# Kernel optimization log

Hardware: AMD Instinct MI355X
Metric: run time of the kernel (lower is better)

The kernel has to match this reference:

```python
import jax, jax.numpy as jnp
import numpy as np

D = 64      # in_feats
OUT = 64    # out_feats
MEM = 4     # mem_size
NREL = 8    # num_rels
N = 20000   # num nodes
E = 50000   # num edges
FF = 16     # dim_feedforward (hardcoded in module)
NH = 4      # nhead (hardcoded)
EPS = 1e-5  # LayerNorm eps (torch default)


def _ln(x, w, b):
    m = x.mean(-1, keepdims=True)
    v = ((x - m) ** 2).mean(-1, keepdims=True)
    return (x - m) * jax.lax.rsqrt(v + EPS) * w + b


def _enc(x, Wqkv, bqkv, Wo, bo, W1, b1, W2, b2, ln1w, ln1b, ln2w, ln2b):
    # torch TransformerEncoderLayer, batch_first, post-norm, eval mode, no padding mask (all-zero mask)
    B, S, d = x.shape
    dh = d // NH
    qkv = x @ Wqkv.T + bqkv
    q, k, v = jnp.split(qkv, 3, axis=-1)
    q = q.reshape(B, S, NH, dh)
    k = k.reshape(B, S, NH, dh)
    v = v.reshape(B, S, NH, dh)
    att = jax.nn.softmax(jnp.einsum('bqhd,bkhd->bhqk', q, k) / jnp.sqrt(jnp.float32(dh)), axis=-1)
    o = jnp.einsum('bhqk,bkhd->bqhd', att, v).reshape(B, S, d) @ Wo.T + bo
    x = _ln(x + o, ln1w, ln1b)
    ff = jax.nn.relu(x @ W1.T + b1) @ W2.T + b2
    return _ln(x + ff, ln2w, ln2b)


def setup_inputs() -> dict:
    key = jax.random.key(0)
    ks = jax.random.split(key, 16)
    s = 0.05
    inp = {
        'feat': jax.random.normal(ks[0], (N, D), jnp.float32),
        'src_idx': jax.random.randint(ks[1], (E,), 0, N),
        'dst_idx': jax.random.randint(ks[2], (E,), 0, N),
        'etype': jax.random.randint(ks[3], (E,), 0, NREL),
        'Wqkv': jax.random.normal(ks[4], (3 * D, D), jnp.float32) * s,
        'bqkv': jnp.zeros((3 * D,), jnp.float32),
        'Wo': jax.random.normal(ks[5], (D, D), jnp.float32) * s,
        'bo': jnp.zeros((D,), jnp.float32),
        'W1': jax.random.normal(ks[6], (FF, D), jnp.float32) * s,
        'b1': jnp.zeros((FF,), jnp.float32),
        'W2': jax.random.normal(ks[7], (D, FF), jnp.float32) * s,
        'b2': jnp.zeros((D,), jnp.float32),
        'ln1w': jnp.ones((D,), jnp.float32),
        'ln1b': jnp.zeros((D,), jnp.float32),
        'ln2w': jnp.ones((D,), jnp.float32),
        'ln2b': jnp.zeros((D,), jnp.float32),
        'Wc': jax.random.normal(ks[8], (MEM, D), jnp.float32) * s,
        'bc': jnp.zeros((MEM,), jnp.float32),
        'CLS': jax.random.normal(ks[9], (MEM, D), jnp.float32),
        'SEP': jax.random.normal(ks[10], (D,), jnp.float32),
        'Wm': jax.random.normal(ks[11], (OUT * D, D), jnp.float32) * s,
        'h_bias': jnp.zeros((OUT,), jnp.float32),
    }
    return inp


def reference(feat, src_idx, dst_idx, etype, Wqkv, bqkv, Wo, bo, W1, b1, W2, b2,
              ln1w, ln1b, ln2w, ln2b, Wc, bc, CLS, SEP, Wm, h_bias):
    enc_args = (Wqkv, bqkv, Wo, bo, W1, b1, W2, b2, ln1w, ln1b, ln2w, ln2b)

    def cls_pass(s_, d_):
        # run the shared encoder MEM times with a different CLS token; the math
        # is identical for every relation type, so no per-etype partition needed
        B = s_.shape[0]
        outs = []
        mem = jnp.zeros((B, D), s_.dtype)
        for i in range(MEM):
            cls = jnp.broadcast_to(CLS[i], (B, D))[:, None, :]
            sep = jnp.broadcast_to(SEP, (B, D))[:, None, :]
            seq = jnp.concatenate([cls, s_[:, None, :], sep, d_[:, None, :]], axis=1)  # [B,4,D]
            t = _enc(seq, *enc_args)[:, 0, :]
            outs.append(t)
            mem = mem + t
        return mem, jnp.stack(outs)  # [B,D], [MEM,B,D]

    src = feat[src_idx]  # [E,D]
    dst = feat[dst_idx]
    mem_emb, tmps = cls_pass(src, dst)
    cat_all = tmps @ Wc.T + bc               # [MEM,E,MEM]
    w = (mem_emb @ Wm.T).reshape(E, OUT, D)  # per-edge hypernetwork weight
    msg = jnp.einsum('eoi,ei->eo', w, src)   # [E,OUT]

    # dgl fn.mean aggregation over destination nodes (0 for isolated nodes)
    cnt = jax.ops.segment_sum(jnp.ones((E,), msg.dtype), dst_idx, num_segments=N)
    agg = jax.ops.segment_sum(msg, dst_idx, num_segments=N)
    node_rep = jnp.where(cnt[:, None] > 0, agg / jnp.maximum(cnt, 1.0)[:, None], 0.0)
    node_rep = node_rep + h_bias

    # self loop (same hypernetwork path over every node)
    mem_s, _ = cls_pass(feat, feat)
    hs = (mem_s @ Wm.T).reshape(N, OUT, D)
    node_rep = node_rep + jnp.einsum('noi,ni->no', hs, feat)

    # reconstruct torch concat order of category/label: outer loop etype, inner loop mem idx
    et = etype.astype(jnp.int32)
    counts = jax.ops.segment_sum(jnp.ones((E,), jnp.int32), etype, num_segments=NREL)
    start = jnp.concatenate([jnp.zeros((1,), jnp.int32), jnp.cumsum(counts)[:-1].astype(jnp.int32)])
    order = jnp.argsort(etype, stable=True)
    rank = jnp.zeros((E,), jnp.int32).at[order].set(jnp.arange(E, dtype=jnp.int32) - start[et[order]])
    base = start[et] * MEM + rank                                            # [E]
    pos = base[None, :] + jnp.arange(MEM, dtype=jnp.int32)[:, None] * counts[et][None, :]  # [MEM,E]
    category = jnp.zeros((MEM * E, MEM), cat_all.dtype).at[pos.reshape(-1)].set(cat_all.reshape(-1, MEM))
    label = jnp.zeros((MEM * E,), jnp.int32).at[pos.reshape(-1)].set(
        jnp.repeat(jnp.arange(MEM, dtype=jnp.int32), E))
    return node_rep, label, category
```

## Files before the change

kernel.cpp:

```cpp
#include <hip/hip_runtime.h>
#include <hip/hip_bf16.h>

typedef float f32x4_t __attribute__((ext_vector_type(4)));
typedef short bf16x8_t __attribute__((ext_vector_type(8)));

#define MFMA(a, b, c) __builtin_amdgcn_mfma_f32_16x16x32_bf16(a, b, c, 0, 0, 0)

#define C_Q0   0
#define C_S00  256
#define C_S02  272
#define C_VCLS 288
#define C_VSEP 544

__device__ __forceinline__ short f2bf(float x) {
    return (short)__builtin_bit_cast(unsigned short, __float2bfloat16(x));
}
__device__ __forceinline__ float bf2f(short s) {
    return __builtin_bit_cast(float, ((unsigned)(unsigned short)s) << 16);
}
__device__ __forceinline__ float head_sum16(float v) {
#pragma unroll
    for (int off = 1; off < 16; off <<= 1) v += __shfl_xor(v, off, 64);
    return v;
}

__global__ void k_prep(const float* __restrict__ Wo, const float* __restrict__ Wqkv,
                       const float* __restrict__ W1, const float* __restrict__ W2,
                       const float* __restrict__ Wm, const float* __restrict__ Wc,
                       const float* __restrict__ bqkv,
                       const float* __restrict__ CLS, const float* __restrict__ SEP,
                       const int* __restrict__ etype, const int* __restrict__ dst,
                       short* __restrict__ Bpack, short* __restrict__ WoP,
                       short* __restrict__ WkvP, short* __restrict__ W1P,
                       short* __restrict__ W2P, short* __restrict__ WcP,
                       float* __restrict__ consts,
                       int* __restrict__ hist, int* __restrict__ cnt, int E)
{
    int bx = blockIdx.x;
    if (bx < 136) {
        int tid = bx * 256 + threadIdx.x;
        short tmp[8];
        if (tid < 32768) {
            int u = tid, lane = u & 63, nt = (u >> 6) & 3, kstep = u >> 8;
            int o = nt * 16 + (lane & 15);
            int kb = kstep * 32 + (lane >> 4) * 8;
#pragma unroll
            for (int t = 0; t < 8; t++) { int k = kb + t; tmp[t] = f2bf(Wm[(o * 64 + (k >> 6)) * 64 + (k & 63)]); }
            *(bf16x8_t*)&Bpack[(size_t)u * 8] = *(bf16x8_t*)tmp;
        } else if (tid < 33280) {
            int u = tid - 32768, lane = u & 63, nt = (u >> 6) & 3, kstep = u >> 8;
            int o = nt * 16 + (lane & 15), kb = kstep * 32 + (lane >> 4) * 8;
#pragma unroll
            for (int t = 0; t < 8; t++) tmp[t] = f2bf(Wo[o * 64 + kb + t]);
            *(bf16x8_t*)&WoP[(size_t)u * 8] = *(bf16x8_t*)tmp;
        } else if (tid < 34304) {
            int u = tid - 33280, lane = u & 63, nt = (u >> 6) & 7, kstep = u >> 9;
            int col = nt * 16 + (lane & 15), kb = kstep * 32 + (lane >> 4) * 8;
            int row = 64 + col;
#pragma unroll
            for (int t = 0; t < 8; t++) tmp[t] = f2bf(Wqkv[row * 64 + kb + t]);
            *(bf16x8_t*)&WkvP[(size_t)u * 8] = *(bf16x8_t*)tmp;
        } else if (tid < 34432) {
            int u = tid - 34304, lane = u & 63, kstep = u >> 6;
            int f = lane & 15, kb = kstep * 32 + (lane >> 4) * 8;
#pragma unroll
            for (int t = 0; t < 8; t++) tmp[t] = f2bf(W1[f * 64 + kb + t]);
            *(bf16x8_t*)&W1P[(size_t)u * 8] = *(bf16x8_t*)tmp;
        } else if (tid < 34688) {
            int u = tid - 34432, lane = u & 63, nt = u >> 6;
            int o = nt * 16 + (lane & 15), kb = (lane >> 4) * 8;
#pragma unroll
            for (int t = 0; t < 8; t++) { int k = kb + t; tmp[t] = (k < 16) ? f2bf(W2[o * 16 + k]) : (short)0; }
            *(bf16x8_t*)&W2P[(size_t)u * 8] = *(bf16x8_t*)tmp;
        } else if (tid < 34816) {
            int u = tid - 34688, lane = u & 63, kstep = u >> 6;
            int m = lane & 15, kb = kstep * 32 + (lane >> 4) * 8;
#pragma unroll
            for (int t = 0; t < 8; t++) tmp[t] = (m < 4) ? f2bf(Wc[m * 64 + kb + t]) : (short)0;
            *(bf16x8_t*)&WcP[(size_t)u * 8] = *(bf16x8_t*)tmp;
        }
    } else if (bx == 136) {
        if (threadIdx.x < 64) {
            int lane = threadIdx.x;
            float ksep = bqkv[64 + lane], vsep = bqkv[128 + lane];
            for (int c = 0; c < 64; c++) {
                float sc = SEP[c];
                ksep += Wqkv[(64 + lane) * 64 + c] * sc;
                vsep += Wqkv[(128 + lane) * 64 + c] * sc;
            }
            consts[C_VSEP + lane] = vsep;
            for (int i = 0; i < 4; i++) {
                float q0 = bqkv[lane], kcls = bqkv[64 + lane], vcls = bqkv[128 + lane];
                for (int c = 0; c < 64; c++) {
                    float cc = CLS[i * 64 + c];
                    q0   += Wqkv[lane * 64 + c] * cc;
                    kcls += Wqkv[(64 + lane) * 64 + c] * cc;
                    vcls += Wqkv[(128 + lane) * 64 + c] * cc;
                }
                consts[C_Q0 + i * 64 + lane] = q0;
                consts[C_VCLS + i * 64 + lane] = vcls;
                float p00 = head_sum16(q0 * kcls) * 0.25f;
                float p02 = head_sum16(q0 * ksep) * 0.25f;
                if ((lane & 15) == 0) {
                    consts[C_S00 + i * 4 + (lane >> 4)] = p00;
                    consts[C_S02 + i * 4 + (lane >> 4)] = p02;
                }
            }
        }
    } else {
        __shared__ int h[8];
        int chunk = bx - 137;
        int tid = threadIdx.x;
        if (tid < 8) h[tid] = 0;
        __syncthreads();
        int e = chunk * 256 + tid;
        if (e < E) {
            atomicAdd(&h[etype[e]], 1);
            atomicAdd(&cnt[dst[e]], 1);
        }
        __syncthreads();
        if (tid < 8) hist[chunk * 8 + tid] = h[tid];
    }
}

__global__ void k_scan(const int* __restrict__ hist, int* __restrict__ chunkoff,
                       int* __restrict__ startg, int* __restrict__ countsg, int nch,
                       const float* __restrict__ consts, const float* __restrict__ Wqkv,
                       const float* __restrict__ bqkv,
                       short* __restrict__ WqkP, float* __restrict__ bqk)
{
    int lane = threadIdx.x;
    int g = lane & 7, seg = lane >> 3;
    int per = (nch + 7) / 8;
    int c0 = seg * per, c1 = c0 + per; if (c1 > nch) c1 = nch;
    int sum = 0;
    for (int c = c0; c < c1; c++) sum += hist[c * 8 + g];
    int pre = 0, tot = 0;
#pragma unroll
    for (int s2 = 0; s2 < 8; s2++) {
        int v = __shfl(sum, s2 * 8 + g, 64);
        tot += v;
        if (s2 < seg) pre += v;
    }
    int run = pre;
    for (int c = c0; c < c1; c++) { chunkoff[c * 8 + g] = run; run += hist[c * 8 + g]; }
    if (seg == 0) {
        countsg[g] = tot;
        int sg = 0;
#pragma unroll
        for (int g2 = 0; g2 < 8; g2++) { int v = __shfl(tot, g2, 64); if (g2 < g) sg += v; }
        startg[g] = sg;
    }

    int ih = lane & 15, ii = ih & 3, hh = ih >> 2;
    int lh8 = (lane >> 4) * 8;
    short tmp[8];
#pragma unroll
    for (int kstep = 0; kstep < 2; kstep++) {
#pragma unroll
        for (int t = 0; t < 8; t++) {
            int k = kstep * 32 + lh8 + t;
            float s = 0.f;
            for (int u = 0; u < 16; u++)
                s += consts[C_Q0 + ii * 64 + hh * 16 + u] * Wqkv[(64 + hh * 16 + u) * 64 + k];
            tmp[t] = f2bf(0.25f * s);
        }
        *(bf16x8_t*)&WqkP[(size_t)(kstep * 64 + lane) * 8] = *(bf16x8_t*)tmp;
    }
    if (lane < 16) {
        float s = 0.f;
        for (int u = 0; u < 16; u++)
            s += consts[C_Q0 + ii * 64 + hh * 16 + u] * bqkv[64 + hh * 16 + u];
        bqk[lane] = 0.25f * s;
    }
}

__global__ __launch_bounds__(256) void k_kv(const float* __restrict__ feat,
        const short* __restrict__ WkvP, const short* __restrict__ WqkP,
        const float* __restrict__ bqkv, const float* __restrict__ bqk,
        float* __restrict__ vnode, float* __restrict__ qs, int N)
{
    __shared__ __align__(16) short sA[64 * 72];
    int tid = threadIdx.x, lane = tid & 63, w = tid >> 6;
    int l15 = lane & 15, lh = lane >> 4;
    int base = blockIdx.x * 64;
#pragma unroll
    for (int rr = 0; rr < 16; rr++) {
        int row = w * 16 + rr;
        int n = base + row; n = n < N ? n : N - 1;
        sA[row * 72 + lane] = f2bf(feat[(size_t)n * 64 + lane]);
    }
    __syncthreads();
    const bf16x8_t* bp = (const bf16x8_t*)WkvP;
    bf16x8_t bv0 = bp[(0 * 8 + 4 + w) * 64 + lane];
    bf16x8_t bv1 = bp[(1 * 8 + 4 + w) * 64 + lane];
    bf16x8_t bq0 = ((const bf16x8_t*)WqkP)[lane];
    bf16x8_t bq1 = ((const bf16x8_t*)WqkP)[64 + lane];
    int kof = lh * 8;
    int col = w * 16 + l15;
    float biasv = bqkv[128 + col];
    float bqv = bqk[l15];
#pragma unroll
    for (int rt = 0; rt < 4; rt++) {
        bf16x8_t a0 = *(const bf16x8_t*)&sA[(rt * 16 + l15) * 72 + kof];
        bf16x8_t a1 = *(const bf16x8_t*)&sA[(rt * 16 + l15) * 72 + 32 + kof];
        f32x4_t av = {0.f, 0.f, 0.f, 0.f};
        av = MFMA(a0, bv0, av); av = MFMA(a1, bv1, av);
#pragma unroll
        for (int r = 0; r < 4; r++) {
            int n = base + rt * 16 + lh * 4 + r;
            if (n < N) vnode[(size_t)n * 64 + col] = av[r] + biasv;
        }
        if (w == 0) {
            f32x4_t aq = {0.f, 0.f, 0.f, 0.f};
            aq = MFMA(a0, bq0, aq); aq = MFMA(a1, bq1, aq);
#pragma unroll
            for (int r = 0; r < 4; r++) {
                int n = base + rt * 16 + lh * 4 + r;
                if (n < N) qs[(size_t)n * 16 + l15] = aq[r] + bqv;
            }
        }
    }
}

struct EncW {
    const float* consts; const float* CLS; const float* bo;
    const float* b1; const float* b2;
    const float* ln1w; const float* ln1b; const float* ln2w; const float* ln2b;
    const short* WoP; const short* W1P; const short* W2P; const short* WcP;
    const float* bc;
};

__global__ __launch_bounds__(256) void k_enc(const int* __restrict__ src_idx,
        const int* __restrict__ dst_idx,
        const float* __restrict__ vnode, const float* __restrict__ qs, EncW W,
        float* __restrict__ mem_out, float* __restrict__ cat_out, int E, int M)
{
    __shared__ __align__(16) short sA[64 * 72];
    __shared__ __align__(16) short sF[64 * 40];
    int tid = threadIdx.x, lane = tid & 63, w = tid >> 6;
    int l15 = lane & 15, lh = lane >> 4;
    int base = blockIdx.x * 16;

#pragma unroll
    for (int z = 0; z < 4; z++) {
        int zz = z * 64 + lane;
        sF[(w * 16 + (zz >> 4)) * 40 + 16 + (zz & 15)] = 0;
    }

    float vclsr[4], s00r[4], s02r[4];
#pragma unroll
    for (int i = 0; i < 4; i++) {
        vclsr[i] = W.consts[C_VCLS + i * 64 + lane];
        s00r[i]  = W.consts[C_S00 + i * 4 + lh];
        s02r[i]  = W.consts[C_S02 + i * 4 + lh];
    }
    float vsep = W.consts[C_VSEP + lane];

#pragma unroll
    for (int el = 0; el < 4; el++) {
        int eloc = w * 4 + el;
        int ge = base + eloc; int gc = ge < M ? ge : M - 1;
        int s, d;
        if (gc < E) { s = src_idx[gc]; d = dst_idx[gc]; }
        else        { s = gc - E; d = s; }
        float vs_ = vnode[(size_t)s * 64 + lane];
        float vd  = vnode[(size_t)d * 64 + lane];
        float4 qh_s = *(const float4*)&qs[(size_t)s * 16 + lh * 4];
        float4 qh_d = *(const float4*)&qs[(size_t)d * 16 + lh * 4];
        float qsv[4] = {qh_s.x, qh_s.y, qh_s.z, qh_s.w};
        float qdv[4] = {qh_d.x, qh_d.y, qh_d.z, qh_d.w};
#pragma unroll
        for (int i = 0; i < 4; i++) {
            float s01 = qsv[i], s03 = qdv[i];
            float s00 = s00r[i], s02 = s02r[i];
            float mx = fmaxf(fmaxf(s00, s01), fmaxf(s02, s03));
            float e0 = __expf(s00 - mx), e1 = __expf(s01 - mx);
            float e2 = __expf(s02 - mx), e3 = __expf(s03 - mx);
            float inv = 1.0f / (e0 + e1 + e2 + e3);
            float att = (e0 * vclsr[i] + e1 * vs_ + e2 * vsep + e3 * vd) * inv;
            sA[(eloc * 4 + i) * 72 + lane] = f2bf(att);
        }
    }

    int arow = (w * 16 + l15) * 72;
    int kof = lh * 8;

    const bf16x8_t* bpo = (const bf16x8_t*)W.WoP;
    f32x4_t ac0 = {0.f,0.f,0.f,0.f}, ac1 = ac0, ac2 = ac0, ac3 = ac0;
#pragma unroll
    for (int kstep = 0; kstep < 2; kstep++) {
        bf16x8_t a = *(const bf16x8_t*)&sA[arow + kstep * 32 + kof];
        ac0 = MFMA(a, bpo[(kstep * 4 + 0) * 64 + lane], ac0);
        ac1 = MFMA(a, bpo[(kstep * 4 + 1) * 64 + lane], ac1);
        ac2 = MFMA(a, bpo[(kstep * 4 + 2) * 64 + lane], ac2);
        ac3 = MFMA(a, bpo[(kstep * 4 + 3) * 64 + lane], ac3);
    }

    float x[4][4], y[4][4];
#pragma unroll
    for (int r = 0; r < 4; r++) { x[0][r] = ac0[r]; x[1][r] = ac1[r]; x[2][r] = ac2[r]; x[3][r] = ac3[r]; }
    float lw1[4], lb1[4];
#pragma unroll
    for (int nt = 0; nt < 4; nt++) {
        float b = W.bo[nt * 16 + l15];
        lw1[nt] = W.ln1w[nt * 16 + l15]; lb1[nt] = W.ln1b[nt * 16 + l15];
#pragma unroll
        for (int r = 0; r < 4; r++) x[nt][r] += b + W.CLS[r * 64 + nt * 16 + l15];
    }
#pragma unroll
    for (int r = 0; r < 4; r++) {
        float sm = head_sum16(x[0][r] + x[1][r] + x[2][r] + x[3][r]);
        float mu = sm * 0.015625f;
        float vv = 0.f;
#pragma unroll
        for (int nt = 0; nt < 4; nt++) { float dd = x[nt][r] - mu; vv = fmaf(dd, dd, vv); }
        vv = head_sum16(vv);
        float rs = rsqrtf(vv * 0.015625f + 1e-5f);
#pragma unroll
        for (int nt = 0; nt < 4; nt++) y[nt][r] = (x[nt][r] - mu) * rs * lw1[nt] + lb1[nt];
    }
#pragma unroll
    for (int nt = 0; nt < 4; nt++)
#pragma unroll
        for (int r = 0; r < 4; r++)
            sA[(w * 16 + lh * 4 + r) * 72 + nt * 16 + l15] = f2bf(y[nt][r]);

    const bf16x8_t* bp1 = (const bf16x8_t*)W.W1P;
    f32x4_t fa = {0.f,0.f,0.f,0.f};
#pragma unroll
    for (int kstep = 0; kstep < 2; kstep++) {
        bf16x8_t a = *(const bf16x8_t*)&sA[arow + kstep * 32 + kof];
        fa = MFMA(a, bp1[kstep * 64 + lane], fa);
    }
    float b1v = W.b1[l15];
#pragma unroll
    for (int r = 0; r < 4; r++)
        sF[(w * 16 + lh * 4 + r) * 40 + l15] = f2bf(fmaxf(fa[r] + b1v, 0.f));

    const bf16x8_t* bp2 = (const bf16x8_t*)W.W2P;
    bf16x8_t af = *(const bf16x8_t*)&sF[(w * 16 + l15) * 40 + kof];
    f32x4_t z0 = {0.f,0.f,0.f,0.f}, z1 = z0, z2 = z0, z3 = z0;
    z0 = MFMA(af, bp2[0 * 64 + lane], z0);
    z1 = MFMA(af, bp2[1 * 64 + lane], z1);
    z2 = MFMA(af, bp2[2 * 64 + lane], z2);
    z3 = MFMA(af, bp2[3 * 64 + lane], z3);

    float t[4][4];
#pragma unroll
    for (int r = 0; r < 4; r++) { x[0][r] = z0[r]; x[1][r] = z1[r]; x[2][r] = z2[r]; x[3][r] = z3[r]; }
    float lw2[4], lb2[4];
#pragma unroll
    for (int nt = 0; nt < 4; nt++) {
        float b = W.b2[nt * 16 + l15];
        lw2[nt] = W.ln2w[nt * 16 + l15]; lb2[nt] = W.ln2b[nt * 16 + l15];
#pragma unroll
        for (int r = 0; r < 4; r++) x[nt][r] += b + y[nt][r];
    }
#pragma unroll
    for (int r = 0; r < 4; r++) {
        float sm = head_sum16(x[0][r] + x[1][r] + x[2][r] + x[3][r]);
        float mu = sm * 0.015625f;
        float vv = 0.f;
#pragma unroll
        for (int nt = 0; nt < 4; nt++) { float dd = x[nt][r] - mu; vv = fmaf(dd, dd, vv); }
        vv = head_sum16(vv);
        float rs = rsqrtf(vv * 0.015625f + 1e-5f);
#pragma unroll
        for (int nt = 0; nt < 4; nt++) t[nt][r] = (x[nt][r] - mu) * rs * lw2[nt] + lb2[nt];
    }

    int eloc = w * 4 + lh, ge = base + eloc;

    if (base < E) {
#pragma unroll
        for (int nt = 0; nt < 4; nt++)
#pragma unroll
            for (int r = 0; r < 4; r++)
                sA[(w * 16 + lh * 4 + r) * 72 + nt * 16 + l15] = f2bf(t[nt][r]);
        const bf16x8_t* bpc = (const bf16x8_t*)W.WcP;
        f32x4_t ca = {0.f,0.f,0.f,0.f};
#pragma unroll
        for (int kstep = 0; kstep < 2; kstep++) {
            bf16x8_t a = *(const bf16x8_t*)&sA[arow + kstep * 32 + kof];
            ca = MFMA(a, bpc[kstep * 64 + lane], ca);
        }
        if (l15 < 4 && ge < E) {
            float bcv = W.bc[l15];
#pragma unroll
            for (int r = 0; r < 4; r++)
                cat_out[((size_t)r * E + ge) * 4 + l15] = ca[r] + bcv;
        }
    }

    if (ge < M) {
#pragma unroll
        for (int nt = 0; nt < 4; nt++)
            mem_out[(size_t)ge * 64 + nt * 16 + l15] = t[nt][0] + t[nt][1] + t[nt][2] + t[nt][3];
    }
}

__global__ __launch_bounds__(256, 3) void k_hyper(
        const float* __restrict__ feat, const int* __restrict__ src_idx,
        const int* __restrict__ dst_idx, const float* __restrict__ memall,
        const short* __restrict__ Bpack,
        float* __restrict__ agg, float* __restrict__ selfm, int E, int M)
{
    __shared__ short xsT[64 * 132];
    __shared__ __align__(16) short sB[2][8192];
    int tid = threadIdx.x, lane = tid & 63, w = tid >> 6;
    int l15 = lane & 15, lh = lane >> 4, koff = lh * 8;
    int base = blockIdx.x * 128;

    const bf16x8_t* bp = (const bf16x8_t*)Bpack;

    auto stage = [&](int c, int buf) {
#pragma unroll
        for (int jj = 0; jj < 4; ++jj) {
            int j = w * 4 + jj;
            int il_ic = j >> 3, q = j & 7;
            const short* src = (const short*)(bp + (size_t)(c * 2 + il_ic) * 512
                                              + (q >> 2) * 256 + (q & 3) * 64 + lane);
            short* dst = &sB[buf][j * 512];
            __builtin_amdgcn_global_load_lds(
                (const __attribute__((address_space(1))) void*)src,
                (__attribute__((address_space(3))) void*)dst, 16, 0, 0);
        }
    };

    stage(0, 0);

    for (int rr = 0; rr < 32; ++rr) {
        int row = w * 32 + rr, gr = base + row;
        float xv = 0.f;
        if (gr < M) {
            int xi = gr < E ? src_idx[gr] : gr - E;
            xv = feat[(size_t)xi * 64 + lane];
        }
        xsT[lane * 132 + row] = f2bf(xv);
    }

    bf16x8_t am[2][2];
#pragma unroll
    for (int tt = 0; tt < 2; ++tt) {
        int gr = base + w * 32 + tt * 16 + l15;
        const float* mp = memall + (size_t)(gr < M ? gr : 0) * 64 + koff;
#pragma unroll
        for (int kk = 0; kk < 2; ++kk)
#pragma unroll
            for (int t = 0; t < 8; ++t)
                am[tt][kk][t] = f2bf(mp[kk * 32 + t]);
    }

    f32x4_t out[2][4];
#pragma unroll
    for (int tt = 0; tt < 2; ++tt)
#pragma unroll
        for (int nt = 0; nt < 4; ++nt) out[tt][nt] = (f32x4_t){0.f, 0.f, 0.f, 0.f};
    const f32x4_t ZERO = {0.f, 0.f, 0.f, 0.f};

    int xrow0 = w * 32 + lh * 4;

    int cur = 0;
    for (int c = 0; c < 32; ++c) {
        if (c + 1 < 32) {
            stage(c + 1, cur ^ 1);
            asm volatile("s_waitcnt vmcnt(4)" ::: "memory");
        } else {
            asm volatile("s_waitcnt vmcnt(0)" ::: "memory");
        }
        __builtin_amdgcn_s_barrier();
#pragma unroll
        for (int ic = 0; ic < 2; ++ic) {
            int i = c * 2 + ic;
            unsigned long long xw0 = *(const unsigned long long*)&xsT[i * 132 + xrow0];
            unsigned long long xw1 = *(const unsigned long long*)&xsT[i * 132 + xrow0 + 16];
            float x0[4], x1[4];
            {
                unsigned lo0 = (unsigned)xw0, hi0 = (unsigned)(xw0 >> 32);
                unsigned lo1 = (unsigned)xw1, hi1 = (unsigned)(xw1 >> 32);
                x0[0] = __builtin_bit_cast(float, lo0 << 16);
                x0[1] = __builtin_bit_cast(float, lo0 & 0xffff0000u);
                x0[2] = __builtin_bit_cast(float, hi0 << 16);
                x0[3] = __builtin_bit_cast(float, hi0 & 0xffff0000u);
                x1[0] = __builtin_bit_cast(float, lo1 << 16);
                x1[1] = __builtin_bit_cast(float, lo1 & 0xffff0000u);
                x1[2] = __builtin_bit_cast(float, hi1 << 16);
                x1[3] = __builtin_bit_cast(float, hi1 & 0xffff0000u);
            }
            const bf16x8_t* bfr = (const bf16x8_t*)&sB[cur][ic * 4096];
            f32x4_t P0[4], P1[4];
            __builtin_amdgcn_s_setprio(1);
#pragma unroll
            for (int nt = 0; nt < 4; ++nt) {
                bf16x8_t B0 = bfr[nt * 64 + lane];
                bf16x8_t B1 = bfr[(4 + nt) * 64 + lane];
                P0[nt] = MFMA(am[0][0], B0, ZERO);
                P1[nt] = MFMA(am[1][0], B0, ZERO);
                P0[nt] = MFMA(am[0][1], B1, P0[nt]);
                P1[nt] = MFMA(am[1][1], B1, P1[nt]);
            }
            __builtin_amdgcn_s_setprio(0);
#pragma unroll
            for (int nt = 0; nt < 4; ++nt)
#pragma unroll
                for (int r = 0; r < 4; ++r) {
                    out[0][nt][r] = fmaf(x0[r], P0[nt][r], out[0][nt][r]);
                    out[1][nt][r] = fmaf(x1[r], P1[nt][r], out[1][nt][r]);
                }
        }
        __builtin_amdgcn_s_barrier();
        cur ^= 1;
    }

#pragma unroll
    for (int tt = 0; tt < 2; ++tt) {
        int orow = w * 32 + tt * 16 + lh * 4;
        int di[4];
#pragma unroll
        for (int r = 0; r < 4; ++r) {
            int grow = base + orow + r;
            di[r] = (grow < E) ? dst_idx[grow] : 0;
        }
#pragma unroll
        for (int nt = 0; nt < 4; ++nt) {
            int o = nt * 16 + l15;
#pragma unroll
            for (int r = 0; r < 4; ++r) {
                int grow = base + orow + r;
                if (grow < M) {
                    float v = out[tt][nt][r];
                    if (grow < E) atomicAdd(&agg[(size_t)di[r] * 64 + o], v);
                    else selfm[(size_t)(grow - E) * 64 + o] = v;
                }
            }
        }
    }
}

__global__ void k_fin(const float* __restrict__ agg, const int* __restrict__ cnt,
                      const float* __restrict__ selfm, const float* __restrict__ h_bias,
                      float* __restrict__ outp, int N)
{
    int t = blockIdx.x * 256 + threadIdx.x;
    if (t < N * 64) {
        int n = t >> 6, o = t & 63;
        int c = cnt[n];
        float av = (c > 0) ? agg[t] / (float)c : 0.f;
        outp[t] = av + h_bias[o] + selfm[t];
    }
}

__global__ __launch_bounds__(256) void k_scatter(const int* __restrict__ etype,
        const float* __restrict__ cat_all,
        const int* __restrict__ chunkoff, const int* __restrict__ startg,
        const int* __restrict__ countsg,
        float* __restrict__ out_label, float* __restrict__ out_cat, int E)
{
    __shared__ int wc[4][8];
    int tid = threadIdx.x, lane = tid & 63, w = tid >> 6;
    int chunk = blockIdx.x;
    int e = chunk * 256 + w * 64 + lane;
    int et = (e < E) ? etype[e] : -1;
    unsigned long long mk[8];
#pragma unroll
    for (int g = 0; g < 8; g++) mk[g] = __ballot(et == g);
    if (lane < 8) wc[w][lane] = (int)__popcll(mk[lane]);
    __syncthreads();
    if (et >= 0) {
        unsigned long long lt = (1ull << lane) - 1ull;
        int myr = chunkoff[chunk * 8 + et] + (int)__popcll(mk[et] & lt);
#pragma unroll
        for (int w2 = 0; w2 < 4; w2++) if (w2 < w) myr += wc[w2][et];
        int sg = startg[et], cg = countsg[et];
        size_t pbase = (size_t)sg * 4 + myr;
#pragma unroll
        for (int i = 0; i < 4; i++) {
            size_t pos = pbase + (size_t)i * cg;
            out_label[pos] = (float)i;
            const float* ca = &cat_all[((size_t)i * E + e) * 4];
            float4 cv = {ca[0], ca[1], ca[2], ca[3]};
            *(float4*)&out_cat[pos * 4] = cv;
        }
    }
}

extern "C" void kernel_launch(void* const* d_in, const int* in_sizes, int n_in,
                              void* d_out, int out_size, void* d_ws, size_t ws_size,
                              hipStream_t stream)
{
    const float* feat    = (const float*)d_in[0];
    const int*   src_idx = (const int*)d_in[1];
    const int*   dst_idx = (const int*)d_in[2];
    const int*   etype   = (const int*)d_in[3];
    const float* Wqkv    = (const float*)d_in[4];
    const float* bqkv    = (const float*)d_in[5];
    const float* Wo      = (const float*)d_in[6];
    const float* bo      = (const float*)d_in[7];
    const float* W1      = (const float*)d_in[8];
    const float* b1      = (const float*)d_in[9];
    const float* W2      = (const float*)d_in[10];
    const float* b2      = (const float*)d_in[11];
    const float* ln1w    = (const float*)d_in[12];
    const float* ln1b    = (const float*)d_in[13];
    const float* ln2w    = (const float*)d_in[14];
    const float* ln2b    = (const float*)d_in[15];
    const float* Wc      = (const float*)d_in[16];
    const float* bc      = (const float*)d_in[17];
    const float* CLS     = (const float*)d_in[18];
    const float* SEP     = (const float*)d_in[19];
    const float* Wm      = (const float*)d_in[20];
    const float* h_bias  = (const float*)d_in[21];

    const int N = in_sizes[0] / 64;
    const int E = in_sizes[1];
    const int M = E + N;
    const int NCH = (E + 255) / 256;

    float* ws = (float*)d_ws;
    size_t off = 0;
    auto alloc = [&](size_t n) { float* p = ws + off; off += (n + 63) & ~(size_t)63; return p; };
    float* qs      = alloc((size_t)N * 16);
    float* vnode   = alloc((size_t)N * 64);
    float* mem_all = alloc((size_t)M * 64);
    float* cat_all = alloc((size_t)E * 16);
    float* agg     = alloc((size_t)N * 64 + N);
    int*   cnt     = (int*)(agg + (size_t)N * 64);
    float* selfm   = alloc((size_t)N * 64);
    float* consts  = alloc(1024);
    short* Bpack   = (short*)alloc(131072);
    short* WoP     = (short*)alloc(2048);
    short* WkvP    = (short*)alloc(4096);
    short* W1P     = (short*)alloc(512);
    short* W2P     = (short*)alloc(1024);
    short* WcP     = (short*)alloc(512);
    short* WqkP    = (short*)alloc(512);
    float* bqk     = alloc(64);
    int*   hist    = (int*)alloc(NCH * 8);
    int*   chunkoff= (int*)alloc(NCH * 8);
    int*   startg  = (int*)alloc(8);
    int*   countsg = (int*)alloc(8);

    float* out_node  = (float*)d_out;
    float* out_label = out_node + (size_t)N * 64;
    float* out_cat   = out_label + (size_t)4 * E;

    hipMemsetAsync(agg, 0, ((size_t)N * 64 + N) * sizeof(float), stream);

    k_prep<<<137 + NCH, 256, 0, stream>>>(Wo, Wqkv, W1, W2, Wm, Wc, bqkv, CLS, SEP,
                                          etype, dst_idx, Bpack, WoP, WkvP, W1P, W2P, WcP,
                                          consts, hist, cnt, E);
    k_scan<<<1, 64, 0, stream>>>(hist, chunkoff, startg, countsg, NCH,
                                 consts, Wqkv, bqkv, WqkP, bqk);

    k_kv<<<(N + 63) / 64, 256, 0, stream>>>(feat, WkvP, WqkP, bqkv, bqk, vnode, qs, N);

    EncW W{consts, CLS, bo, b1, b2, ln1w, ln1b, ln2w, ln2b, WoP, W1P, W2P, WcP, bc};

    k_enc<<<(M + 15) / 16, 256, 0, stream>>>(src_idx, dst_idx, vnode, qs, W,
                                             mem_all, cat_all, E, M);

    k_hyper<<<(M + 127) / 128, 256, 0, stream>>>(feat, src_idx, dst_idx, mem_all, Bpack,
                                                 agg, selfm, E, M);

    k_fin<<<(N * 64 + 255) / 256, 256, 0, stream>>>(agg, cnt, selfm, h_bias, out_node, N);

    k_scatter<<<NCH, 256, 0, stream>>>(etype, cat_all, chunkoff, startg, countsg,
                                       out_label, out_cat, E);
}
```

Baseline: 150.9 us.

## Retile hypernetwork GEMM across 2x2 waves and fuse finalize with scatter

The k_hyper wave tiling changes from each wave owning 32 rows by all 64 output columns to a 2x2 arrangement, where each wave owns 64 rows by 32 columns. Each wave now reads only half the B fragments from LDS per step and reuses each one across four row tiles. In exchange it holds twice as many A fragments in registers, and a __syncthreads is added after the xsT fill. Separately, the k_fin and k_scatter kernels are merged into one launch that dispatches on block index, saving one kernel launch.

```diff
diff --git a/kernel.cpp b/kernel.cpp
--- a/kernel.cpp
+++ b/kernel.cpp
@@ -410,6 +410,7 @@
     __shared__ __align__(16) short sB[2][8192];
     int tid = threadIdx.x, lane = tid & 63, w = tid >> 6;
     int l15 = lane & 15, lh = lane >> 4, koff = lh * 8;
+    int rw = w >> 1, cw = w & 1;
     int base = blockIdx.x * 128;
 
     const bf16x8_t* bp = (const bf16x8_t*)Bpack;
@@ -440,10 +441,10 @@
         xsT[lane * 132 + row] = f2bf(xv);
     }
 
-    bf16x8_t am[2][2];
-#pragma unroll
-    for (int tt = 0; tt < 2; ++tt) {
-        int gr = base + w * 32 + tt * 16 + l15;
+    bf16x8_t am[4][2];
+#pragma unroll
+    for (int tt = 0; tt < 4; ++tt) {
+        int gr = base + rw * 64 + tt * 16 + l15;
         const float* mp = memall + (size_t)(gr < M ? gr : 0) * 64 + koff;
 #pragma unroll
         for (int kk = 0; kk < 2; ++kk)
@@ -452,14 +453,17 @@
                 am[tt][kk][t] = f2bf(mp[kk * 32 + t]);
     }
 
-    f32x4_t out[2][4];
-#pragma unroll
-    for (int tt = 0; tt < 2; ++tt)
-#pragma unroll
-        for (int nt = 0; nt < 4; ++nt) out[tt][nt] = (f32x4_t){0.f, 0.f, 0.f, 0.f};
+    f32x4_t out[4][2];
+#pragma unroll
+    for (int tt = 0; tt < 4; ++tt)
+#pragma unroll
+        for (int n2 = 0; n2 < 2; ++n2) out[tt][n2] = (f32x4_t){0.f, 0.f, 0.f, 0.f};
     const f32x4_t ZERO = {0.f, 0.f, 0.f, 0.f};
 
-    int xrow0 = w * 32 + lh * 4;
+    int xrow0 = rw * 64 + lh * 4;
+    int nt0 = cw * 2, nt1 = cw * 2 + 1;
+
+    __syncthreads();
 
     int cur = 0;
     for (int c = 0; c < 32; ++c) {
@@ -473,49 +477,46 @@
 #pragma unroll
         for (int ic = 0; ic < 2; ++ic) {
             int i = c * 2 + ic;
-            unsigned long long xw0 = *(const unsigned long long*)&xsT[i * 132 + xrow0];
-            unsigned long long xw1 = *(const unsigned long long*)&xsT[i * 132 + xrow0 + 16];
-            float x0[4], x1[4];
-            {
-                unsigned lo0 = (unsigned)xw0, hi0 = (unsigned)(xw0 >> 32);
-                unsigned lo1 = (unsigned)xw1, hi1 = (unsigned)(xw1 >> 32);
-                x0[0] = __builtin_bit_cast(float, lo0 << 16);
-                x0[1] = __builtin_bit_cast(float, lo0 & 0xffff0000u);
-                x0[2] = __builtin_bit_cast(float, hi0 << 16);
-                x0[3] = __builtin_bit_cast(float, hi0 & 0xffff0000u);
-                x1[0] = __builtin_bit_cast(float, lo1 << 16);
-                x1[1] = __builtin_bit_cast(float, lo1 & 0xffff0000u);
-                x1[2] = __builtin_bit_cast(float, hi1 << 16);
-                x1[3] = __builtin_bit_cast(float, hi1 & 0xffff0000u);
+            float xv[4][4];
+#pragma unroll
+            for (int tt = 0; tt < 4; ++tt) {
+                unsigned long long xw = *(const unsigned long long*)&xsT[i * 132 + xrow0 + tt * 16];
+                unsigned lo = (unsigned)xw, hi = (unsigned)(xw >> 32);
+                xv[tt][0] = __builtin_bit_cast(float, lo << 16);
+                xv[tt][1] = __builtin_bit_cast(float, lo & 0xffff0000u);
+                xv[tt][2] = __builtin_bit_cast(float, hi << 16);
+                xv[tt][3] = __builtin_bit_cast(float, hi & 0xffff0000u);
             }
             const bf16x8_t* bfr = (const bf16x8_t*)&sB[cur][ic * 4096];
-            f32x4_t P0[4], P1[4];
+            bf16x8_t B00 = bfr[nt0 * 64 + lane];
+            bf16x8_t B01 = bfr[nt1 * 64 + lane];
+            bf16x8_t B10 = bfr[(4 + nt0) * 64 + lane];
+            bf16x8_t B11 = bfr[(4 + nt1) * 64 + lane];
+            f32x4_t P[4][2];
             __builtin_amdgcn_s_setprio(1);
 #pragma unroll
-            for (int nt = 0; nt < 4; ++nt) {
-                bf16x8_t B0 = bfr[nt * 64 + lane];
-                bf16x8_t B1 = bfr[(4 + nt) * 64 + lane];
-                P0[nt] = MFMA(am[0][0], B0, ZERO);
-                P1[nt] = MFMA(am[1][0], B0, ZERO);
-                P0[nt] = MFMA(am[0][1], B1, P0[nt]);
-                P1[nt] = MFMA(am[1][1], B1, P1[nt]);
+            for (int tt = 0; tt < 4; ++tt) {
+                P[tt][0] = MFMA(am[tt][0], B00, ZERO);
+                P[tt][1] = MFMA(am[tt][0], B01, ZERO);
+                P[tt][0] = MFMA(am[tt][1], B10, P[tt][0]);
+                P[tt][1] = MFMA(am[tt][1], B11, P[tt][1]);
             }
             __builtin_amdgcn_s_setprio(0);
 #pragma unroll
-            for (int nt = 0; nt < 4; ++nt)
-#pragma unroll
-                for (int r = 0; r < 4; ++r) {
-                    out[0][nt][r] = fmaf(x0[r], P0[nt][r], out[0][nt][r]);
-                    out[1][nt][r] = fmaf(x1[r], P1[nt][r], out[1][nt][r]);
-                }
+            for (int tt = 0; tt < 4; ++tt)
+#pragma unroll
+                for (int n2 = 0; n2 < 2; ++n2)
+#pragma unroll
+                    for (int r = 0; r < 4; ++r)
+                        out[tt][n2][r] = fmaf(xv[tt][r], P[tt][n2][r], out[tt][n2][r]);
         }
         __builtin_amdgcn_s_barrier();
         cur ^= 1;
     }
 
 #pragma unroll
-    for (int tt = 0; tt < 2; ++tt) {
-        int orow = w * 32 + tt * 16 + lh * 4;
+    for (int tt = 0; tt < 4; ++tt) {
+        int orow = rw * 64 + tt * 16 + lh * 4;
         int di[4];
 #pragma unroll
         for (int r = 0; r < 4; ++r) {
@@ -523,13 +524,13 @@
             di[r] = (grow < E) ? dst_idx[grow] : 0;
         }
 #pragma unroll
-        for (int nt = 0; nt < 4; ++nt) {
-            int o = nt * 16 + l15;
+        for (int n2 = 0; n2 < 2; ++n2) {
+            int o = (cw * 2 + n2) * 16 + l15;
 #pragma unroll
             for (int r = 0; r < 4; ++r) {
                 int grow = base + orow + r;
                 if (grow < M) {
-                    float v = out[tt][nt][r];
+                    float v = out[tt][n2][r];
                     if (grow < E) atomicAdd(&agg[(size_t)di[r] * 64 + o], v);
                     else selfm[(size_t)(grow - E) * 64 + o] = v;
                 }
@@ -538,49 +539,49 @@
     }
 }
 
-__global__ void k_fin(const float* __restrict__ agg, const int* __restrict__ cnt,
-                      const float* __restrict__ selfm, const float* __restrict__ h_bias,
-                      float* __restrict__ outp, int N)
-{
-    int t = blockIdx.x * 256 + threadIdx.x;
-    if (t < N * 64) {
-        int n = t >> 6, o = t & 63;
-        int c = cnt[n];
-        float av = (c > 0) ? agg[t] / (float)c : 0.f;
-        outp[t] = av + h_bias[o] + selfm[t];
-    }
-}
-
-__global__ __launch_bounds__(256) void k_scatter(const int* __restrict__ etype,
-        const float* __restrict__ cat_all,
+__global__ __launch_bounds__(256) void k_finsc(
+        const float* __restrict__ agg, const int* __restrict__ cnt,
+        const float* __restrict__ selfm, const float* __restrict__ h_bias,
+        float* __restrict__ outp, int N,
+        const int* __restrict__ etype, const float* __restrict__ cat_all,
         const int* __restrict__ chunkoff, const int* __restrict__ startg,
         const int* __restrict__ countsg,
-        float* __restrict__ out_label, float* __restrict__ out_cat, int E)
+        float* __restrict__ out_label, float* __restrict__ out_cat, int E, int FB)
 {
-    __shared__ int wc[4][8];
-    int tid = threadIdx.x, lane = tid & 63, w = tid >> 6;
-    int chunk = blockIdx.x;
-    int e = chunk * 256 + w * 64 + lane;
-    int et = (e < E) ? etype[e] : -1;
-    unsigned long long mk[8];
-#pragma unroll
-    for (int g = 0; g < 8; g++) mk[g] = __ballot(et == g);
-    if (lane < 8) wc[w][lane] = (int)__popcll(mk[lane]);
-    __syncthreads();
-    if (et >= 0) {
-        unsigned long long lt = (1ull << lane) - 1ull;
-        int myr = chunkoff[chunk * 8 + et] + (int)__popcll(mk[et] & lt);
-#pragma unroll
-        for (int w2 = 0; w2 < 4; w2++) if (w2 < w) myr += wc[w2][et];
-        int sg = startg[et], cg = countsg[et];
-        size_t pbase = (size_t)sg * 4 + myr;
-#pragma unroll
-        for (int i = 0; i < 4; i++) {
-            size_t pos = pbase + (size_t)i * cg;
-            out_label[pos] = (float)i;
-            const float* ca = &cat_all[((size_t)i * E + e) * 4];
-            float4 cv = {ca[0], ca[1], ca[2], ca[3]};
-            *(float4*)&out_cat[pos * 4] = cv;
+    if ((int)blockIdx.x < FB) {
+        int t = blockIdx.x * 256 + threadIdx.x;
+        if (t < N * 64) {
+            int n = t >> 6, o = t & 63;
+            int c = cnt[n];
+            float av = (c > 0) ? agg[t] / (float)c : 0.f;
+            outp[t] = av + h_bias[o] + selfm[t];
+        }
+    } else {
+        __shared__ int wc[4][8];
+        int tid = threadIdx.x, lane = tid & 63, w = tid >> 6;
+        int chunk = blockIdx.x - FB;
+        int e = chunk * 256 + w * 64 + lane;
+        int et = (e < E) ? etype[e] : -1;
+        unsigned long long mk[8];
+#pragma unroll
+        for (int g = 0; g < 8; g++) mk[g] = __ballot(et == g);
+        if (lane < 8) wc[w][lane] = (int)__popcll(mk[lane]);
+        __syncthreads();
+        if (et >= 0) {
+            unsigned long long lt = (1ull << lane) - 1ull;
+            int myr = chunkoff[chunk * 8 + et] + (int)__popcll(mk[et] & lt);
+#pragma unroll
+            for (int w2 = 0; w2 < 4; w2++) if (w2 < w) myr += wc[w2][et];
+            int sg = startg[et], cg = countsg[et];
+            size_t pbase = (size_t)sg * 4 + myr;
+#pragma unroll
+            for (int i = 0; i < 4; i++) {
+                size_t pos = pbase + (size_t)i * cg;
+                out_label[pos] = (float)i;
+                const float* ca = &cat_all[((size_t)i * E + e) * 4];
+                float4 cv = {ca[0], ca[1], ca[2], ca[3]};
+                *(float4*)&out_cat[pos * 4] = cv;
+            }
         }
     }
 }
@@ -616,6 +617,7 @@
     const int E = in_sizes[1];
     const int M = E + N;
     const int NCH = (E + 255) / 256;
+    const int FB = (N * 64 + 255) / 256;
 
     float* ws = (float*)d_ws;
     size_t off = 0;
@@ -663,8 +665,7 @@
     k_hyper<<<(M + 127) / 128, 256, 0, stream>>>(feat, src_idx, dst_idx, mem_all, Bpack,
                                                  agg, selfm, E, M);
 
-    k_fin<<<(N * 64 + 255) / 256, 256, 0, stream>>>(agg, cnt, selfm, h_bias, out_node, N);
-
-    k_scatter<<<NCH, 256, 0, stream>>>(etype, cat_all, chunkoff, startg, countsg,
-                                       out_label, out_cat, E);
-}
+    k_finsc<<<FB + NCH, 256, 0, stream>>>(agg, cnt, selfm, h_bias, out_node, N,
+                                          etype, cat_all, chunkoff, startg, countsg,
+                                          out_label, out_cat, E, FB);
+}
```

Measured after the change: 162.1 us. +7.4%, slower.
